# Kernel optimization log

Measured on AMD Instinct MI355X. Metric: run time of the kernel, lower is better.

The kernel has to match this reference:

```python
import jax, jax.numpy as jnp
import numpy as np
from jax import lax

DIM = 512
NUM_HEADS = 8
RANK = 4
SR = 2
LN_EPS = 1e-5


def setup_inputs() -> dict:
    key = jax.random.key(0)
    ks = jax.random.split(key, 16)
    B, N, C = 8, 1024, DIM
    H = W = 32
    r = C // RANK  # 128 low-rank bottleneck
    std = 0.02
    x = jax.random.normal(ks[0], (B, N, C), dtype=jnp.float32)
    # training-path random mask: rand > sparsity(=0.5), True = masked out
    mask = jax.random.bernoulli(ks[1], 0.5, (B, NUM_HEADS, N, (H // SR) * (W // SR)))
    # low-rank QKV projection weights, torch Linear layout (out, in), no bias
    q_w1 = jax.random.normal(ks[2], (r, C), dtype=jnp.float32) * std
    q_w2 = jax.random.normal(ks[3], (C, r), dtype=jnp.float32) * std
    k_w1 = jax.random.normal(ks[4], (r, C), dtype=jnp.float32) * std
    k_w2 = jax.random.normal(ks[5], (C, r), dtype=jnp.float32) * std
    v_w1 = jax.random.normal(ks[6], (r, C), dtype=jnp.float32) * std
    v_w2 = jax.random.normal(ks[7], (C, r), dtype=jnp.float32) * std
    # depthwise sr conv: torch Conv2d(dim, dim, k=SR, stride=SR, groups=dim) -> (C,1,SR,SR)
    fan_out = SR * SR * C // C  # = SR*SR
    sr_w = jax.random.normal(ks[8], (C, 1, SR, SR), dtype=jnp.float32) * np.sqrt(2.0 / fan_out)
    sr_b = jnp.zeros((C,), dtype=jnp.float32)
    ln_g = jnp.ones((C,), dtype=jnp.float32)
    ln_b = jnp.zeros((C,), dtype=jnp.float32)
    proj_w = jax.random.normal(ks[9], (C, C), dtype=jnp.float32) * std
    proj_b = jnp.zeros((C,), dtype=jnp.float32)
    return {"x": x, "mask": mask, "q_w1": q_w1, "q_w2": q_w2, "k_w1": k_w1,
            "k_w2": k_w2, "v_w1": v_w1, "v_w2": v_w2, "sr_w": sr_w, "sr_b": sr_b,
            "ln_g": ln_g, "ln_b": ln_b, "proj_w": proj_w, "proj_b": proj_b,
            "H": H, "W": W}


def reference(x, mask, q_w1, q_w2, k_w1, k_w2, v_w1, v_w2, sr_w, sr_b,
              ln_g, ln_b, proj_w, proj_b, H, W):
    B, N, C = x.shape
    hd = C // NUM_HEADS
    scale = hd ** -0.5
    # low-rank q projection
    q = (x @ q_w1.T) @ q_w2.T  # (B,N,C)
    q = q.reshape(B, N, NUM_HEADS, hd).transpose(0, 2, 1, 3)  # (B,h,N,d)
    # spatial reduction: depthwise conv k=stride=SR, then LayerNorm
    x_ = x.transpose(0, 2, 1).reshape(B, C, H, W)
    x_ = lax.conv_general_dilated(x_, sr_w, (SR, SR), 'VALID',
                                  feature_group_count=C,
                                  dimension_numbers=('NCHW', 'OIHW', 'NCHW'))
    x_ = x_ + sr_b[None, :, None, None]
    x_ = x_.reshape(B, C, -1).transpose(0, 2, 1)  # (B, N_new, C)
    mu = jnp.mean(x_, axis=-1, keepdims=True)
    var = jnp.mean(jnp.square(x_ - mu), axis=-1, keepdims=True)
    x_ = (x_ - mu) / jnp.sqrt(var + LN_EPS) * ln_g + ln_b
    Nn = x_.shape[1]
    k = ((x_ @ k_w1.T) @ k_w2.T).reshape(B, Nn, NUM_HEADS, hd).transpose(0, 2, 1, 3)
    v = ((x_ @ v_w1.T) @ v_w2.T).reshape(B, Nn, NUM_HEADS, hd).transpose(0, 2, 1, 3)
    # masked scaled dot-product attention (training path: random mask -> -inf)
    attn = jnp.einsum('bhnd,bhmd->bhnm', q, k) * scale
    attn = jnp.where(mask, -jnp.inf, attn)
    attn = jax.nn.softmax(attn, axis=-1)
    out = jnp.einsum('bhnm,bhmd->bhnd', attn, v)  # (B,h,N,d)
    out = out.transpose(0, 2, 1, 3).reshape(B, N, C)
    out = out @ proj_w.T + proj_b
    return out
```

## Files before the change

### kernel.cpp

```cpp
#include <hip/hip_runtime.h>
#include <hip/hip_bf16.h>
#include <math.h>
#include <stdint.h>

#define DIMC   512
#define NHEAD  8
#define HD     64
#define NTOK   1024
#define MTOK   256
#define BSZ    8
#define LN_EPS 1e-5f

typedef __attribute__((ext_vector_type(8))) short  short8v;
typedef __attribute__((ext_vector_type(4))) float  f32x4;
typedef __attribute__((ext_vector_type(4))) unsigned short us4;

typedef const __attribute__((address_space(1))) unsigned int* gas1_t;
typedef __attribute__((address_space(3))) unsigned int*       las3_t;

__device__ __forceinline__ void gload_lds16(const void* g, void* l) {
    __builtin_amdgcn_global_load_lds((gas1_t)g, (las3_t)l, 16, 0, 0);
}

__device__ __forceinline__ unsigned short f2bf(float f) {
    union { float f; unsigned int u; } v; v.f = f;
    unsigned int u = v.u;
    return (unsigned short)((u + 0x7FFFu + ((u >> 16) & 1u)) >> 16);
}

__global__ void detect_mask_kernel(const unsigned int* __restrict__ m,
                                   int* __restrict__ flag)
{
    if (blockIdx.x == 0 && threadIdx.x == 0) {
        int all01 = 1, allf = 1;
        for (int i = 0; i < 64; ++i) {
            unsigned int w = m[i];
            if (w > 1u) all01 = 0;
            if (w != 0u && w != 0x3F800000u) allf = 0;
        }
        *flag = all01 ? 0 : (allf ? 2 : 1);
    }
}

__global__ __launch_bounds__(256)
void pack_mask_kernel(const void* __restrict__ maskp, const int* __restrict__ flag,
                      unsigned long long* __restrict__ packed)
{
    const int w = threadIdx.x >> 6, lane = threadIdx.x & 63;
    const long long row = (long long)blockIdx.x * 4 + w;
    const int mtype = *flag;
    int m0, m1, m2, m3;
    if (mtype == 0) {
        const int4 v = ((const int4*)maskp)[row * 64 + lane];
        m0 = v.x; m1 = v.y; m2 = v.z; m3 = v.w;
    } else if (mtype == 1) {
        const uchar4 v = ((const uchar4*)maskp)[row * 64 + lane];
        m0 = v.x; m1 = v.y; m2 = v.z; m3 = v.w;
    } else {
        const float4 v = ((const float4*)maskp)[row * 64 + lane];
        m0 = (v.x != 0.f); m1 = (v.y != 0.f); m2 = (v.z != 0.f); m3 = (v.w != 0.f);
    }
    const unsigned long long b0 = __ballot(m0 != 0);
    const unsigned long long b1 = __ballot(m1 != 0);
    const unsigned long long b2 = __ballot(m2 != 0);
    const unsigned long long b3 = __ballot(m3 != 0);
    if (lane < 4) {
        const unsigned long long v = lane == 0 ? b0 : lane == 1 ? b1
                                   : lane == 2 ? b2 : b3;
        packed[row * 4 + lane] = v;
    }
}

__global__ __launch_bounds__(256)
void f32_to_bf16_kernel(const float* __restrict__ in, unsigned short* __restrict__ out,
                        int n4)
{
    for (int i = blockIdx.x * 256 + threadIdx.x; i < n4; i += gridDim.x * 256) {
        const float4 v = ((const float4*)in)[i];
        us4 p;
        p[0] = f2bf(v.x); p[1] = f2bf(v.y); p[2] = f2bf(v.z); p[3] = f2bf(v.w);
        ((us4*)out)[i] = p;
    }
}

__global__ __launch_bounds__(256)
void convert_weights_kernel(const float* __restrict__ qw1, const float* __restrict__ kw1,
                            const float* __restrict__ vw1, const float* __restrict__ qw2,
                            const float* __restrict__ kw2, const float* __restrict__ vw2,
                            const float* __restrict__ pw,  unsigned short* __restrict__ out,
                            unsigned short* __restrict__ w1t)
{
    const int e = (blockIdx.x * 256 + threadIdx.x) * 4;
    const float* src; int off;
    if      (e < 65536)  { src = qw1; off = e; }
    else if (e < 131072) { src = kw1; off = e - 65536; }
    else if (e < 196608) { src = vw1; off = e - 131072; }
    else if (e < 262144) { src = qw2; off = e - 196608; }
    else if (e < 327680) { src = kw2; off = e - 262144; }
    else if (e < 393216) { src = vw2; off = e - 327680; }
    else                 { src = pw;  off = e - 393216; }
    const float4 v = *(const float4*)(src + off);
    us4 p;
    p[0] = f2bf(v.x); p[1] = f2bf(v.y); p[2] = f2bf(v.z); p[3] = f2bf(v.w);
    *(us4*)(out + e) = p;
    if (e < 196608) {
        const int mat = e >> 16, rem = e & 65535;
        const int k = rem >> 9, j = rem & 511;
#pragma unroll
        for (int t = 0; t < 4; ++t)
            w1t[mat * 65536 + (j + t) * 128 + k] = p[t];
    }
}

template<int OUT_MODE, int BSEL>
__global__ __launch_bounds__(256)
void gemm_bf16(const unsigned short* __restrict__ A,
               const unsigned short* __restrict__ B,
               const float* __restrict__ bias,
               void* __restrict__ Cp, int M, int N, int K)
{
    __shared__ unsigned short As[128 * 64];
    __shared__ unsigned short Bs[128 * 64];

    const int tid  = threadIdx.x;
    const int w    = tid >> 6;
    const int lane = tid & 63;
    const int c16  = lane & 15;
    const int g    = lane >> 4;
    const int wr   = w >> 1, wc = w & 1;
    const size_t bm = (size_t)blockIdx.y * 128;
    const size_t bn = (size_t)blockIdx.x * 128;
    if (BSEL) B += (bm >> 9) * 65536;

    f32x4 acc[4][4];
#pragma unroll
    for (int i = 0; i < 4; ++i)
#pragma unroll
        for (int j = 0; j < 4; ++j) acc[i][j] = (f32x4){0.f, 0.f, 0.f, 0.f};

    for (int kt = 0; kt < K; kt += 64) {
        __syncthreads();
#pragma unroll
        for (int i = 0; i < 4; ++i) {
            const int o   = (((i * 4 + w) * 64) + lane) * 16;
            const int row = o >> 7;
            const int col = (o & 127) >> 1;
            gload_lds16(A + (bm + row) * K + kt + col, (char*)As + o);
        }
#pragma unroll
        for (int i = 0; i < 4; ++i) {
            const int o   = (((i * 4 + w) * 64) + lane) * 16;
            const int row = o >> 7;
            const int col = (o & 127) >> 1;
            gload_lds16(B + (bn + row) * K + kt + col, (char*)Bs + o);
        }
        __syncthreads();
#pragma unroll
        for (int kk = 0; kk < 2; ++kk) {
            short8v a[4], bb[4];
#pragma unroll
            for (int mf = 0; mf < 4; ++mf)
                a[mf] = *(const short8v*)(As + (wr * 64 + mf * 16 + c16) * 64 + kk * 32 + g * 8);
#pragma unroll
            for (int nf = 0; nf < 4; ++nf)
                bb[nf] = *(const short8v*)(Bs + (wc * 64 + nf * 16 + c16) * 64 + kk * 32 + g * 8);
#pragma unroll
            for (int mf = 0; mf < 4; ++mf)
#pragma unroll
                for (int nf = 0; nf < 4; ++nf)
                    acc[mf][nf] = __builtin_amdgcn_mfma_f32_16x16x32_bf16(a[mf], bb[nf], acc[mf][nf], 0, 0, 0);
        }
    }

#pragma unroll
    for (int mf = 0; mf < 4; ++mf) {
#pragma unroll
        for (int nf = 0; nf < 4; ++nf) {
            const size_t col = bn + wc * 64 + nf * 16 + c16;
            const size_t r0  = bm + wr * 64 + mf * 16 + g * 4;
            if (OUT_MODE == 0) {
                float* C = (float*)Cp;
                const float bv = (bias != nullptr) ? bias[col] : 0.f;
#pragma unroll
                for (int r = 0; r < 4; ++r)
                    C[(r0 + r) * N + col] = acc[mf][nf][r] + bv;
            } else if (OUT_MODE == 1) {
                unsigned short* C = (unsigned short*)Cp;
#pragma unroll
                for (int r = 0; r < 4; ++r)
                    C[(r0 + r) * N + col] = f2bf(acc[mf][nf][r]);
            } else if (OUT_MODE == 2) {
                unsigned short* C = (unsigned short*)Cp;
                const size_t b  = r0 >> 8;
                const size_t m0 = r0 & 255;
                us4 p;
                p[0] = f2bf(acc[mf][nf][0]); p[1] = f2bf(acc[mf][nf][1]);
                p[2] = f2bf(acc[mf][nf][2]); p[3] = f2bf(acc[mf][nf][3]);
                *(us4*)(C + (b * N + col) * 256 + m0) = p;
            } else {
                if (col < 512) {
                    unsigned short* Ck = (unsigned short*)Cp;
#pragma unroll
                    for (int r = 0; r < 4; ++r)
                        Ck[(r0 + r) * 512 + col] = f2bf(acc[mf][nf][r]);
                } else {
                    unsigned short* Cv = (unsigned short*)Cp + 1048576;
                    const size_t b  = r0 >> 8;
                    const size_t m0 = r0 & 255;
                    us4 p;
                    p[0] = f2bf(acc[mf][nf][0]); p[1] = f2bf(acc[mf][nf][1]);
                    p[2] = f2bf(acc[mf][nf][2]); p[3] = f2bf(acc[mf][nf][3]);
                    *(us4*)(Cv + (b * 512 + (col - 512)) * 256 + m0) = p;
                }
            }
        }
    }
}

__global__ __launch_bounds__(512)
void conv_ln_kernel(const float* __restrict__ x, const float* __restrict__ srw,
                    const float* __restrict__ srb, const float* __restrict__ lng,
                    const float* __restrict__ lnb, unsigned short* __restrict__ xr)
{
    const int c  = threadIdx.x;
    const int bn = blockIdx.x;
    const int b  = bn >> 8;
    const int np = bn & 255;
    const int ho = np >> 4, wo = np & 15;
    const int n00 = (ho * 2) * 32 + wo * 2;

    const float* xb = x + ((size_t)b * NTOK) * DIMC + c;
    const float4 w = *(const float4*)(srw + c * 4);
    float y = srb[c]
            + xb[(size_t)(n00     ) * DIMC] * w.x
            + xb[(size_t)(n00 + 1 ) * DIMC] * w.y
            + xb[(size_t)(n00 + 32) * DIMC] * w.z
            + xb[(size_t)(n00 + 33) * DIMC] * w.w;

    float s = y, s2 = y * y;
#pragma unroll
    for (int off = 32; off > 0; off >>= 1) {
        s  += __shfl_down(s,  off);
        s2 += __shfl_down(s2, off);
    }
    __shared__ float red[16];
    __shared__ float stats[2];
    const int lane = c & 63, wid = c >> 6;
    if (lane == 0) { red[wid] = s; red[8 + wid] = s2; }
    __syncthreads();
    if (c == 0) {
        float ts = 0.f, ts2 = 0.f;
#pragma unroll
        for (int i = 0; i < 8; ++i) { ts += red[i]; ts2 += red[8 + i]; }
        const float mu  = ts * (1.f / 512.f);
        const float var = ts2 * (1.f / 512.f) - mu * mu;
        stats[0] = mu;
        stats[1] = rsqrtf(var + LN_EPS);
    }
    __syncthreads();
    const float mu = stats[0], rstd = stats[1];
    xr[((size_t)(b * MTOK + np)) * DIMC + c] = f2bf((y - mu) * rstd * lng[c] + lnb[c]);
}

__global__ __launch_bounds__(256)
void attn_mfma(const unsigned short* __restrict__ qb,
               const unsigned short* __restrict__ kb,
               const unsigned short* __restrict__ vt,
               const unsigned long long* __restrict__ pmask,
               unsigned short* __restrict__ ob)
{
    __shared__ unsigned short plds[4 * 16 * 256];

    const int tid  = threadIdx.x;
    const int w    = tid >> 6;
    const int lane = tid & 63;
    const int g    = lane >> 4;
    const int c16  = lane & 15;
    const int bh   = blockIdx.x & 63;
    const int qt   = blockIdx.x >> 6;
    const int b    = bh >> 3;
    const int h    = bh & 7;
    const int q0   = qt * 64 + w * 16;

    const size_t prow = (size_t)bh * NTOK + q0 + g * 4;
    unsigned mlo[4], mhi[4];
#pragma unroll
    for (int r = 0; r < 4; ++r) {
        const unsigned long long pm = pmask[(prow + r) * 4 + (c16 & 3)] >> (c16 >> 2);
        mlo[r] = (unsigned)pm;
        mhi[r] = (unsigned)(pm >> 32);
    }

    short8v qf[2];
#pragma unroll
    for (int ks = 0; ks < 2; ++ks)
        qf[ks] = *(const short8v*)(qb + ((size_t)(b * NTOK + q0 + c16)) * DIMC
                                      + h * HD + ks * 32 + g * 8);

    f32x4 s[16];
#pragma unroll
    for (int nf = 0; nf < 16; ++nf) s[nf] = (f32x4){0.f, 0.f, 0.f, 0.f};

#pragma unroll
    for (int nf = 0; nf < 16; ++nf) {
#pragma unroll
        for (int ks = 0; ks < 2; ++ks) {
            const short8v kf = *(const short8v*)(kb + ((size_t)(b * MTOK + nf * 16 + c16)) * DIMC
                                                    + h * HD + ks * 32 + g * 8);
            s[nf] = __builtin_amdgcn_mfma_f32_16x16x32_bf16(qf[ks], kf, s[nf], 0, 0, 0);
        }
    }

    const float scale = 0.125f;
#pragma unroll
    for (int nf = 0; nf < 16; ++nf) {
#pragma unroll
        for (int r = 0; r < 4; ++r) {
            const unsigned bit = ((nf < 8 ? (mlo[r] >> (nf * 4))
                                          : (mhi[r] >> ((nf - 8) * 4))) & 1u);
            s[nf][r] = bit ? -INFINITY : s[nf][r] * scale;
        }
    }

    float mx[4] = {-1e30f, -1e30f, -1e30f, -1e30f};
#pragma unroll
    for (int nf = 0; nf < 16; ++nf)
#pragma unroll
        for (int r = 0; r < 4; ++r) mx[r] = fmaxf(mx[r], s[nf][r]);
#pragma unroll
    for (int off = 8; off >= 1; off >>= 1)
#pragma unroll
        for (int r = 0; r < 4; ++r) mx[r] = fmaxf(mx[r], __shfl_xor(mx[r], off, 64));

    float sm[4] = {0.f, 0.f, 0.f, 0.f};
#pragma unroll
    for (int nf = 0; nf < 16; ++nf)
#pragma unroll
        for (int r = 0; r < 4; ++r) {
            const float p = __expf(s[nf][r] - mx[r]);
            s[nf][r] = p;
            sm[r] += p;
        }
#pragma unroll
    for (int off = 8; off >= 1; off >>= 1)
#pragma unroll
        for (int r = 0; r < 4; ++r) sm[r] += __shfl_xor(sm[r], off, 64);
    float inv[4];
#pragma unroll
    for (int r = 0; r < 4; ++r) inv[r] = 1.0f / sm[r];

    unsigned short* pw = plds + w * 16 * 256;
#pragma unroll
    for (int nf = 0; nf < 16; ++nf) {
        const int key = nf * 16 + c16;
#pragma unroll
        for (int r = 0; r < 4; ++r) {
            const int row = g * 4 + r;
            pw[row * 256 + (key ^ ((row & 7) << 3))] = f2bf(s[nf][r] * inv[r]);
        }
    }

    f32x4 o[4];
#pragma unroll
    for (int df = 0; df < 4; ++df) o[df] = (f32x4){0.f, 0.f, 0.f, 0.f};

    const int prw = c16;
    const unsigned short* pr = pw + prw * 256;
#pragma unroll
    for (int kf = 0; kf < 8; ++kf) {
        const int k0 = kf * 32 + g * 8;
        const short8v pa = *(const short8v*)(pr + (k0 ^ ((prw & 7) << 3)));
#pragma unroll
        for (int df = 0; df < 4; ++df) {
            const short8v vf = *(const short8v*)(vt + ((size_t)(b * DIMC + h * HD + df * 16 + c16)) * MTOK + k0);
            o[df] = __builtin_amdgcn_mfma_f32_16x16x32_bf16(pa, vf, o[df], 0, 0, 0);
        }
    }

#pragma unroll
    for (int df = 0; df < 4; ++df)
#pragma unroll
        for (int r = 0; r < 4; ++r)
            ob[((size_t)(b * NTOK + q0 + g * 4 + r)) * DIMC + h * HD + df * 16 + c16] =
                f2bf(o[df][r]);
}

extern "C" void kernel_launch(void* const* d_in, const int* in_sizes, int n_in,
                              void* d_out, int out_size, void* d_ws, size_t ws_size,
                              hipStream_t stream)
{
    const float* x      = (const float*)d_in[0];
    const void*  mask   = d_in[1];
    const float* q_w1   = (const float*)d_in[2];
    const float* q_w2   = (const float*)d_in[3];
    const float* k_w1   = (const float*)d_in[4];
    const float* k_w2   = (const float*)d_in[5];
    const float* v_w1   = (const float*)d_in[6];
    const float* v_w2   = (const float*)d_in[7];
    const float* sr_w   = (const float*)d_in[8];
    const float* sr_b   = (const float*)d_in[9];
    const float* ln_g   = (const float*)d_in[10];
    const float* ln_b   = (const float*)d_in[11];
    const float* proj_w = (const float*)d_in[12];
    const float* proj_b = (const float*)d_in[13];

    unsigned char* wsb = (unsigned char*)d_ws;
    unsigned short* xb16 = (unsigned short*)(wsb + 0);
    unsigned short* ao16 = (unsigned short*)(wsb + 0);
    unsigned short* qb16 = (unsigned short*)(wsb + (8u  << 20));
    unsigned short* xrb  = (unsigned short*)(wsb + (16u << 20));
    unsigned short* w1t  = (unsigned short*)(wsb + (18u << 20));
    unsigned short* kb16 = (unsigned short*)(wsb + (19u << 20));
    unsigned short* vt16 = (unsigned short*)(wsb + (21u << 20));
    unsigned short* wts  = (unsigned short*)(wsb + (23u << 20));
    unsigned short* wc16 = (unsigned short*)(wsb + (25u << 20));
    unsigned long long* pmask = (unsigned long long*)(wsb + (27u << 20));
    int*            flag = (int*)(wsb + (29u << 20));

    const int QW2 = 196608, PW = 393216;

    detect_mask_kernel<<<1, 1, 0, stream>>>((const unsigned int*)mask, flag);
    pack_mask_kernel<<<16384, 256, 0, stream>>>(mask, flag, pmask);
    convert_weights_kernel<<<640, 256, 0, stream>>>(q_w1, k_w1, v_w1, q_w2, k_w2, v_w2,
                                                    proj_w, wts, w1t);
    f32_to_bf16_kernel<<<2048, 256, 0, stream>>>(x, xb16, 1048576);
    conv_ln_kernel<<<2048, 512, 0, stream>>>(x, sr_w, sr_b, ln_g, ln_b, xrb);

    gemm_bf16<1, 1><<<dim3(4, 12), 256, 0, stream>>>(wts + QW2, w1t, nullptr, wc16, 1536, 512, 128);

    gemm_bf16<1, 0><<<dim3(4, 64), 256, 0, stream>>>(xb16, wc16, nullptr, qb16, 8192, 512, 512);

    gemm_bf16<3, 0><<<dim3(8, 16), 256, 0, stream>>>(xrb, wc16 + 262144, nullptr, kb16, 2048, 1024, 512);

    attn_mfma<<<1024, 256, 0, stream>>>(qb16, kb16, vt16, pmask, ao16);

    gemm_bf16<0, 0><<<dim3(4, 64), 256, 0, stream>>>(ao16, wts + PW, proj_b, d_out, 8192, 512, 512);
}
```

Before: 240.9 us.

## Double-buffer GEMM LDS loads, stage K tile in LDS for attention, parallelize mask detect

```diff
diff --git a/kernel.cpp b/kernel.cpp
--- a/kernel.cpp
+++ b/kernel.cpp
@@ -31,15 +31,11 @@
 __global__ void detect_mask_kernel(const unsigned int* __restrict__ m,
                                    int* __restrict__ flag)
 {
-    if (blockIdx.x == 0 && threadIdx.x == 0) {
-        int all01 = 1, allf = 1;
-        for (int i = 0; i < 64; ++i) {
-            unsigned int w = m[i];
-            if (w > 1u) all01 = 0;
-            if (w != 0u && w != 0x3F800000u) allf = 0;
-        }
-        *flag = all01 ? 0 : (allf ? 2 : 1);
-    }
+    const int lane = threadIdx.x & 63;
+    const unsigned int w = m[lane];
+    const unsigned long long not01 = __ballot(w > 1u);
+    const unsigned long long notf  = __ballot(w != 0u && w != 0x3F800000u);
+    if (lane == 0) *flag = (not01 == 0ull) ? 0 : ((notf == 0ull) ? 2 : 1);
 }
 
 __global__ __launch_bounds__(256)
@@ -119,8 +115,8 @@
                const float* __restrict__ bias,
                void* __restrict__ Cp, int M, int N, int K)
 {
-    __shared__ unsigned short As[128 * 64];
-    __shared__ unsigned short Bs[128 * 64];
+    __shared__ unsigned short As[2][128 * 64];
+    __shared__ unsigned short Bs[2][128 * 64];
 
     const int tid  = threadIdx.x;
     const int w    = tid >> 6;
@@ -138,38 +134,52 @@
 #pragma unroll
         for (int j = 0; j < 4; ++j) acc[i][j] = (f32x4){0.f, 0.f, 0.f, 0.f};
 
-    for (int kt = 0; kt < K; kt += 64) {
-        __syncthreads();
+    const int NT = K >> 6;
+
+    auto stage = [&](int buf, int kt) {
 #pragma unroll
         for (int i = 0; i < 4; ++i) {
             const int o   = (((i * 4 + w) * 64) + lane) * 16;
             const int row = o >> 7;
             const int col = (o & 127) >> 1;
-            gload_lds16(A + (bm + row) * K + kt + col, (char*)As + o);
+            gload_lds16(A + (bm + row) * K + kt + col, (char*)As[buf] + o);
         }
 #pragma unroll
         for (int i = 0; i < 4; ++i) {
             const int o   = (((i * 4 + w) * 64) + lane) * 16;
             const int row = o >> 7;
             const int col = (o & 127) >> 1;
-            gload_lds16(B + (bn + row) * K + kt + col, (char*)Bs + o);
-        }
-        __syncthreads();
+            gload_lds16(B + (bn + row) * K + kt + col, (char*)Bs[buf] + o);
+        }
+    };
+
+    stage(0, 0);
+    int cur = 0;
+    for (int t = 0; t < NT; ++t) {
+        if (t + 1 < NT) {
+            stage(cur ^ 1, (t + 1) * 64);
+            asm volatile("s_waitcnt vmcnt(8)" ::: "memory");
+        } else {
+            asm volatile("s_waitcnt vmcnt(0)" ::: "memory");
+        }
+        asm volatile("s_barrier" ::: "memory");
 #pragma unroll
         for (int kk = 0; kk < 2; ++kk) {
             short8v a[4], bb[4];
 #pragma unroll
             for (int mf = 0; mf < 4; ++mf)
-                a[mf] = *(const short8v*)(As + (wr * 64 + mf * 16 + c16) * 64 + kk * 32 + g * 8);
+                a[mf] = *(const short8v*)(&As[cur][(wr * 64 + mf * 16 + c16) * 64 + kk * 32 + g * 8]);
 #pragma unroll
             for (int nf = 0; nf < 4; ++nf)
-                bb[nf] = *(const short8v*)(Bs + (wc * 64 + nf * 16 + c16) * 64 + kk * 32 + g * 8);
+                bb[nf] = *(const short8v*)(&Bs[cur][(wc * 64 + nf * 16 + c16) * 64 + kk * 32 + g * 8]);
 #pragma unroll
             for (int mf = 0; mf < 4; ++mf)
 #pragma unroll
                 for (int nf = 0; nf < 4; ++nf)
                     acc[mf][nf] = __builtin_amdgcn_mfma_f32_16x16x32_bf16(a[mf], bb[nf], acc[mf][nf], 0, 0, 0);
         }
+        asm volatile("s_barrier" ::: "memory");
+        cur ^= 1;
     }
 
 #pragma unroll
@@ -189,14 +199,6 @@
 #pragma unroll
                 for (int r = 0; r < 4; ++r)
                     C[(r0 + r) * N + col] = f2bf(acc[mf][nf][r]);
-            } else if (OUT_MODE == 2) {
-                unsigned short* C = (unsigned short*)Cp;
-                const size_t b  = r0 >> 8;
-                const size_t m0 = r0 & 255;
-                us4 p;
-                p[0] = f2bf(acc[mf][nf][0]); p[1] = f2bf(acc[mf][nf][1]);
-                p[2] = f2bf(acc[mf][nf][2]); p[3] = f2bf(acc[mf][nf][3]);
-                *(us4*)(C + (b * N + col) * 256 + m0) = p;
             } else {
                 if (col < 512) {
                     unsigned short* Ck = (unsigned short*)Cp;
@@ -262,14 +264,14 @@
     xr[((size_t)(b * MTOK + np)) * DIMC + c] = f2bf((y - mu) * rstd * lng[c] + lnb[c]);
 }
 
-__global__ __launch_bounds__(256)
+__global__ __launch_bounds__(256, 4)
 void attn_mfma(const unsigned short* __restrict__ qb,
                const unsigned short* __restrict__ kb,
                const unsigned short* __restrict__ vt,
                const unsigned long long* __restrict__ pmask,
                unsigned short* __restrict__ ob)
 {
-    __shared__ unsigned short plds[4 * 16 * 256];
+    __shared__ unsigned short Ks[16384];
 
     const int tid  = threadIdx.x;
     const int w    = tid >> 6;
@@ -282,6 +284,17 @@
     const int h    = bh & 7;
     const int q0   = qt * 64 + w * 16;
 
+    const unsigned short* kgb = kb + ((size_t)b * MTOK) * DIMC + h * HD;
+#pragma unroll
+    for (int t = 0; t < 8; ++t) {
+        const int chunk = t * 256 + w * 64 + lane;
+        const int o_dma = chunk * 16;
+        const int row   = o_dma >> 7;
+        const int o_log = o_dma ^ ((row & 7) << 4);
+        const int slot  = (o_log >> 4) & 7;
+        gload_lds16(kgb + (size_t)row * DIMC + slot * 8, (char*)Ks + o_dma);
+    }
+
     const size_t prow = (size_t)bh * NTOK + q0 + g * 4;
     unsigned mlo[4], mhi[4];
 #pragma unroll
@@ -290,23 +303,26 @@
         mlo[r] = (unsigned)pm;
         mhi[r] = (unsigned)(pm >> 32);
     }
-
     short8v qf[2];
 #pragma unroll
     for (int ks = 0; ks < 2; ++ks)
         qf[ks] = *(const short8v*)(qb + ((size_t)(b * NTOK + q0 + c16)) * DIMC
                                       + h * HD + ks * 32 + g * 8);
 
+    asm volatile("s_waitcnt vmcnt(0)" ::: "memory");
+    asm volatile("s_barrier" ::: "memory");
+
     f32x4 s[16];
 #pragma unroll
     for (int nf = 0; nf < 16; ++nf) s[nf] = (f32x4){0.f, 0.f, 0.f, 0.f};
-
 #pragma unroll
     for (int nf = 0; nf < 16; ++nf) {
+        const int kr = nf * 16 + c16;
+        const int sw = (kr & 7) << 4;
 #pragma unroll
         for (int ks = 0; ks < 2; ++ks) {
-            const short8v kf = *(const short8v*)(kb + ((size_t)(b * MTOK + nf * 16 + c16)) * DIMC
-                                                    + h * HD + ks * 32 + g * 8);
+            const int o = (kr << 7) + ks * 64 + g * 16;
+            const short8v kf = *(const short8v*)((const char*)Ks + (o ^ sw));
             s[nf] = __builtin_amdgcn_mfma_f32_16x16x32_bf16(qf[ks], kf, s[nf], 0, 0, 0);
         }
     }
@@ -349,7 +365,9 @@
 #pragma unroll
     for (int r = 0; r < 4; ++r) inv[r] = 1.0f / sm[r];
 
-    unsigned short* pw = plds + w * 16 * 256;
+    asm volatile("s_barrier" ::: "memory");
+
+    unsigned short* pw = Ks + w * 4096;
 #pragma unroll
     for (int nf = 0; nf < 16; ++nf) {
         const int key = nf * 16 + c16;
@@ -419,7 +437,7 @@
 
     const int QW2 = 196608, PW = 393216;
 
-    detect_mask_kernel<<<1, 1, 0, stream>>>((const unsigned int*)mask, flag);
+    detect_mask_kernel<<<1, 64, 0, stream>>>((const unsigned int*)mask, flag);
     pack_mask_kernel<<<16384, 256, 0, stream>>>(mask, flag, pmask);
     convert_weights_kernel<<<640, 256, 0, stream>>>(q_w1, k_w1, v_w1, q_w2, k_w2, v_w2,
                                                     proj_w, wts, w1t);
```

Measured after the change: 220.6 us. 1.09x faster.
